# Optimization experiments

Hardware: AMD Instinct MI355X
Metric: run time of the kernel (lower is better)

Reference implementation:

```python
import jax, jax.numpy as jnp
import numpy as np

DIM = 768   # embedding dim
NH = 12     # num heads
HD = DIM // NH  # head dim = 64
WS = 14     # window size
EPS = 1e-5  # nn.LayerNorm default


def _ln(x, w, b):
    m = jnp.mean(x, -1, keepdims=True)
    v = jnp.var(x, -1, keepdims=True)
    return (x - m) * jax.lax.rsqrt(v + EPS) * w + b


def setup_inputs() -> dict:
    key = jax.random.key(0)
    ks = jax.random.split(key, 8)
    def n(k, shape, s=0.02):
        return jax.random.normal(k, shape, jnp.float32) * s
    return {
        "x": jax.random.normal(ks[0], (4, 64, 64, DIM), jnp.float32),
        "ln1_w": jnp.ones((DIM,), jnp.float32),
        "ln1_b": jnp.zeros((DIM,), jnp.float32),
        "qkv_w": n(ks[1], (DIM, 3 * DIM)),
        "qkv_b": jnp.zeros((3 * DIM,), jnp.float32),
        "proj_w": n(ks[2], (DIM, DIM)),
        "proj_b": jnp.zeros((DIM,), jnp.float32),
        "rel_pos_h": n(ks[3], (2 * WS - 1, HD)),
        "rel_pos_w": n(ks[4], (2 * WS - 1, HD)),
        "ln2_w": jnp.ones((DIM,), jnp.float32),
        "ln2_b": jnp.zeros((DIM,), jnp.float32),
        "fc1_w": n(ks[5], (DIM, 4 * DIM)),
        "fc1_b": jnp.zeros((4 * DIM,), jnp.float32),
        "fc2_w": n(ks[6], (4 * DIM, DIM)),
        "fc2_b": jnp.zeros((DIM,), jnp.float32),
    }


def _block(x, ln1_w, ln1_b, qkv_w, qkv_b, proj_w, proj_b,
           rel_pos_h, rel_pos_w, ln2_w, ln2_b, fc1_w, fc1_b, fc2_w, fc2_b):
    B, H, W, C = x.shape
    shortcut = x
    xn = _ln(x, ln1_w, ln1_b)

    # ---- window partition (pad H,W up to multiples of WS) ----
    pad_h = (-H) % WS
    pad_w = (-W) % WS
    xp = jnp.pad(xn, ((0, 0), (0, pad_h), (0, pad_w), (0, 0)))
    Hp, Wp = H + pad_h, W + pad_w
    nh, nw = Hp // WS, Wp // WS
    xw = xp.reshape(B, nh, WS, nw, WS, C).transpose(0, 1, 3, 2, 4, 5)
    xw = xw.reshape(B * nh * nw, WS, WS, C)  # [Bw, ws, ws, C]
    Bw = B * nh * nw
    N = WS * WS

    # ---- attention with decomposed relative position bias ----
    qkv = xw.reshape(Bw, N, C) @ qkv_w + qkv_b            # [Bw, N, 3C]
    qkv = qkv.reshape(Bw, N, 3, NH, HD).transpose(2, 0, 3, 1, 4)  # [3, Bw, NH, N, HD]
    q, k, v = qkv[0], qkv[1], qkv[2]
    scale = HD ** -0.5
    attn = jnp.einsum("bhnd,bhmd->bhnm", q * scale, k)    # [Bw, NH, N, N]

    # decomposed rel pos: Rh[q_h, k_h, c], Rw[q_w, k_w, c]
    idx = jnp.arange(WS)[:, None] - jnp.arange(WS)[None, :] + (WS - 1)
    Rh = rel_pos_h[idx]  # [ws, ws, HD]
    Rw = rel_pos_w[idx]  # [ws, ws, HD]
    rq = q.reshape(Bw, NH, WS, WS, HD)
    rel_h = jnp.einsum("bnhwc,hkc->bnhwk", rq, Rh)  # over q rows vs k rows
    rel_w = jnp.einsum("bnhwc,wkc->bnhwk", rq, Rw)  # over q cols vs k cols
    attn = (attn.reshape(Bw, NH, WS, WS, WS, WS)
            + rel_h[..., :, None] + rel_w[..., None, :]).reshape(Bw, NH, N, N)

    attn = jax.nn.softmax(attn, axis=-1)
    out = jnp.einsum("bhnm,bhmd->bhnd", attn, v)          # [Bw, NH, N, HD]
    out = out.transpose(0, 2, 1, 3).reshape(Bw, WS, WS, C)
    out = out @ proj_w + proj_b

    # ---- window unpartition + crop padding ----
    out = out.reshape(B, nh, nw, WS, WS, C).transpose(0, 1, 3, 2, 4, 5)
    out = out.reshape(B, Hp, Wp, C)[:, :H, :W, :]

    x = shortcut + out

    # ---- MLP ----
    h = _ln(x, ln2_w, ln2_b)
    h = jax.nn.gelu(h @ fc1_w + fc1_b, approximate=False)
    x = x + (h @ fc2_w + fc2_b)
    return x


def reference(x, ln1_w, ln1_b, qkv_w, qkv_b, proj_w, proj_b,
              rel_pos_h, rel_pos_w, ln2_w, ln2_b, fc1_w, fc1_b, fc2_w, fc2_b):
    return _block(x, ln1_w, ln1_b, qkv_w, qkv_b, proj_w, proj_b,
                  rel_pos_h, rel_pos_w, ln2_w, ln2_b, fc1_w, fc1_b, fc2_w, fc2_b)
```

## Files before the change

kernel.cpp:

```cpp
#include <hip/hip_runtime.h>

typedef unsigned short u16;
typedef __bf16 bf16x8_t __attribute__((ext_vector_type(8)));
typedef float f32x4_t __attribute__((ext_vector_type(4)));

__device__ __forceinline__ float bf2f(u16 u) {
    union { unsigned u; float f; } c; c.u = ((unsigned)u) << 16; return c.f;
}
__device__ __forceinline__ u16 f2bf(float f) {
    union { float f; unsigned u; } c; c.f = f;
    unsigned u = c.u;
    unsigned r = (u + 0x7FFFu + ((u >> 16) & 1u)) >> 16;
    return (u16)r;
}

__device__ __forceinline__ void gld16(const u16* g, u16* l) {
    __builtin_amdgcn_global_load_lds(
        (const __attribute__((address_space(1))) unsigned*)g,
        (__attribute__((address_space(3))) unsigned*)l, 16, 0, 0);
}

__device__ __forceinline__ void block_sum2(float& s, float& sq) {
    for (int o = 32; o > 0; o >>= 1) { s += __shfl_xor(s, o); sq += __shfl_xor(sq, o); }
    __shared__ float sh[8];
    int wid = threadIdx.x >> 6;
    if ((threadIdx.x & 63) == 0) { sh[wid] = s; sh[4 + wid] = sq; }
    __syncthreads();
    s  = sh[0] + sh[1] + sh[2] + sh[3];
    sq = sh[4] + sh[5] + sh[6] + sh[7];
}

__global__ __launch_bounds__(256) void ln1_window(
    const float* __restrict__ x, const float* __restrict__ w, const float* __restrict__ b,
    u16* __restrict__ out, int row0)
{
    int lrow = blockIdx.x, tid = threadIdx.x;
    int wr = row0 + lrow;
    int wb = wr / 196, t = wr % 196;
    int gh = ((wb % 25) / 5) * 14 + t / 14;
    int gw = (wb % 5) * 14 + t % 14;
    size_t orow = (size_t)lrow * 768;
    __shared__ u16 rowbuf[768];
    if (gh >= 64 || gw >= 64) {
        rowbuf[tid] = 0; rowbuf[tid + 256] = 0; rowbuf[tid + 512] = 0;
        __syncthreads();
        if (tid < 96) *(uint4*)&out[orow + (tid << 3)] = *(const uint4*)&rowbuf[tid << 3];
        return;
    }
    size_t base = (size_t)(((wb / 25) * 64 + gh) * 64 + gw) * 768;
    float v0 = x[base + tid], v1 = x[base + tid + 256], v2 = x[base + tid + 512];
    float s = v0 + v1 + v2, sq = v0 * v0 + v1 * v1 + v2 * v2;
    block_sum2(s, sq);
    float mean = s * (1.0f / 768.0f);
    float var  = sq * (1.0f / 768.0f) - mean * mean;
    float inv  = rsqrtf(var + 1e-5f);
    rowbuf[tid]       = f2bf((v0 - mean) * inv * w[tid]       + b[tid]);
    rowbuf[tid + 256] = f2bf((v1 - mean) * inv * w[tid + 256] + b[tid + 256]);
    rowbuf[tid + 512] = f2bf((v2 - mean) * inv * w[tid + 512] + b[tid + 512]);
    __syncthreads();
    if (tid < 96) *(uint4*)&out[orow + (tid << 3)] = *(const uint4*)&rowbuf[tid << 3];
}

__global__ __launch_bounds__(256) void ln2_chunk(
    const float* __restrict__ xin, const float* __restrict__ w, const float* __restrict__ b,
    u16* __restrict__ out)
{
    int row = blockIdx.x, tid = threadIdx.x;
    size_t base = (size_t)row * 768;
    __shared__ u16 rowbuf[768];
    float v0 = xin[base + tid], v1 = xin[base + tid + 256], v2 = xin[base + tid + 512];
    float s = v0 + v1 + v2, sq = v0 * v0 + v1 * v1 + v2 * v2;
    block_sum2(s, sq);
    float mean = s * (1.0f / 768.0f);
    float var  = sq * (1.0f / 768.0f) - mean * mean;
    float inv  = rsqrtf(var + 1e-5f);
    rowbuf[tid]       = f2bf((v0 - mean) * inv * w[tid]       + b[tid]);
    rowbuf[tid + 256] = f2bf((v1 - mean) * inv * w[tid + 256] + b[tid + 256]);
    rowbuf[tid + 512] = f2bf((v2 - mean) * inv * w[tid + 512] + b[tid + 512]);
    __syncthreads();
    if (tid < 96) *(uint4*)&out[base + (tid << 3)] = *(const uint4*)&rowbuf[tid << 3];
}

__global__ __launch_bounds__(256) void transpose_wf(
    const float* __restrict__ in, u16* __restrict__ out, int K, int N)
{
    __shared__ u16 t[32][33];
    __shared__ u16 tt[32][32];
    int n0 = blockIdx.x * 32, k0 = blockIdx.y * 32;
    int tx = threadIdx.x & 31, ty = threadIdx.x >> 5;
    for (int q = 0; q < 4; q++) {
        int k = k0 + ty + q * 8, n = n0 + tx;
        t[ty + q * 8][tx] = (k < K && n < N) ? f2bf(in[(size_t)k * N + n]) : (u16)0;
    }
    __syncthreads();
    for (int q = 0; q < 4; q++) tt[ty + q * 8][tx] = t[tx][ty + q * 8];
    __syncthreads();
    if (threadIdx.x < 128) {
        int r = threadIdx.x >> 2, c8 = (threadIdx.x & 3) << 3;
        int n = n0 + r, k = k0 + c8;
        if (n < N && k < K)
            *(uint4*)&out[(size_t)n * K + k] = *(const uint4*)&tt[r][c8];
    }
}

__global__ __launch_bounds__(256) void build_relT(
    const float* __restrict__ rh, const float* __restrict__ rw, u16* __restrict__ out)
{
    int i = blockIdx.x * 256 + threadIdx.x;
    int r = i >> 6, c = i & 63;
    float v = (r < 27) ? rh[r * 64 + c] : (r < 54 ? rw[(r - 27) * 64 + c] : 0.f);
    out[i] = f2bf(v);
}

__global__ __launch_bounds__(256) void build_vt(
    const u16* __restrict__ qkvc, u16* __restrict__ vt)
{
    int z = blockIdx.x;
    int wb = z / 12, h = z % 12;
    __shared__ u16 t[64][232];
    int tid = threadIdx.x;
    for (int base = 0; base < 196; base += 4) {
        int m = base + (tid >> 6);
        int d = tid & 63;
        t[d][m] = qkvc[(size_t)(wb * 196 + m) * 2304 + 1536 + h * 64 + d];
    }
    for (int idx = tid; idx < 28 * 64; idx += 256) {
        int m = 196 + idx / 64, d = idx % 64;
        t[d][m] = 0;
    }
    __syncthreads();
    size_t ob = (size_t)z * 64 * 224;
    for (int idx = tid; idx < 64 * 28; idx += 256) {
        int d = idx / 28, c8 = (idx % 28) << 3;
        *(uint4*)&vt[ob + (size_t)d * 224 + c8] = *(const uint4*)&t[d][c8];
    }
}

__global__ __launch_bounds__(256) void softmax_rel2(
    u16* __restrict__ S, const u16* __restrict__ G2)
{
    int z = blockIdx.y;
    int wv = threadIdx.x >> 6, lane = threadIdx.x & 63;
    int n = blockIdx.x * 4 + wv;
    size_t srow = (size_t)z * 196 * 224 + (size_t)n * 224;
    const u16* g2 = G2 + (size_t)z * 196 * 64 + (size_t)n * 64;
    int qh = n / 14, qw = n % 14;
    float s[4];
    for (int c = 0; c < 4; c++) {
        int m = c * 64 + lane;
        if (m < 196) {
            int kk = m / 14, jj = m % 14;
            float bh = bf2f(g2[qh - kk + 13]);
            float bw = bf2f(g2[27 + qw - jj + 13]);
            s[c] = 0.125f * bf2f(S[srow + m]) + bh + bw;
        } else s[c] = -1e30f;
    }
    float mx = fmaxf(fmaxf(s[0], s[1]), fmaxf(s[2], s[3]));
    for (int o = 32; o > 0; o >>= 1) mx = fmaxf(mx, __shfl_xor(mx, o));
    float e[4], sm = 0.f;
    for (int c = 0; c < 4; c++) {
        int m = c * 64 + lane;
        e[c] = (m < 196) ? expf(s[c] - mx) : 0.f;
        sm += e[c];
    }
    for (int o = 32; o > 0; o >>= 1) sm += __shfl_xor(sm, o);
    float inv = 1.0f / sm;
    for (int c = 0; c < 4; c++) {
        int m = c * 64 + lane;
        if (m < 224) S[srow + m] = f2bf(e[c] * inv);
    }
}

__device__ __forceinline__ int swz_off(int row, int kcElem) {
    return row * 32 + (kcElem ^ (((row >> 1) & 3) << 3));
}

template <int MODE>
__global__ __launch_bounds__(256, 4) void gemm_nt(
    const u16* __restrict__ Aall, const u16* __restrict__ Ball,
    const float* __restrict__ bias, const float* xf,
    u16* __restrict__ Cb, float* Cf, int M, int row0)
{
    constexpr int BK = 32;
    int N, K, lda, ldb;
    size_t aoff = 0, boff = 0, coff = 0;
    if constexpr (MODE == 0) { N = 2304; K = 768; lda = 768; ldb = 768; }
    else if constexpr (MODE == 1) {
        N = 196; K = 64; lda = 2304; ldb = 2304;
        int z = blockIdx.z;
        aoff = (size_t)(z / 12) * 196 * 2304 + (size_t)(z % 12) * 64;
        boff = aoff + 768;
        coff = (size_t)z * 196 * 224;
    } else if constexpr (MODE == 2) {
        N = 64; K = 224; lda = 224; ldb = 224;
        int z = blockIdx.z;
        aoff = (size_t)z * 196 * 224;
        boff = (size_t)z * 64 * 224;
        coff = (size_t)(z / 12) * 196 * 768 + (size_t)(z % 12) * 64;
    } else if constexpr (MODE == 3) { N = 768; K = 768; lda = 768; ldb = 768; }
    else if constexpr (MODE == 4) { N = 3072; K = 768; lda = 768; ldb = 768; }
    else if constexpr (MODE == 6) {
        N = 64; K = 64; lda = 2304; ldb = 64;
        int z = blockIdx.z;
        aoff = (size_t)(z / 12) * 196 * 2304 + (size_t)(z % 12) * 64;
        boff = 0;
        coff = (size_t)z * 196 * 64;
    }
    else { N = 768; K = 3072; lda = 3072; ldb = 3072; }

    __shared__ __align__(16) u16 smem[16384];

    int tid = threadIdx.x, wid = tid >> 6, lane = tid & 63;
    int quad = lane >> 4, l16 = lane & 15;

    int bx = blockIdx.x, by = blockIdx.y;
    if constexpr (MODE != 1 && MODE != 2 && MODE != 6) {
        int gX = gridDim.x;
        int nwg = gX * gridDim.y;
        int orig = by * gX + bx;
        int q = nwg >> 3, r = nwg & 7;
        int xcd = orig & 7, idx = orig >> 3;
        int wg = (xcd < r ? xcd * (q + 1) : r * (q + 1) + (xcd - r) * q) + idx;
        bx = wg % gX; by = wg / gX;
    }
    int m_tile = by * 128, n_tile = bx * 128;
    int wm0 = (wid >> 1) * 64, wn0 = (wid & 1) * 64;

    const u16* A = Aall + aoff;
    const u16* B = Ball + boff;

    const u16* gA[2]; const u16* gB[2];
    int loff[2];
    {
        int s = lane & 3, rofs = lane >> 2;
        for (int j = 0; j < 2; j++) {
            int r0 = wid * 32 + j * 16;
            int rr = r0 + rofs;
            int xr = (rr >> 1) & 3;
            int colo = ((s ^ xr) << 3);
            int am = m_tile + rr; if (am > M - 1) am = M - 1;
            int bn = n_tile + rr; if (bn > N - 1) bn = N - 1;
            gA[j] = A + (size_t)am * lda + colo;
            gB[j] = B + (size_t)bn * ldb + colo;
            loff[j] = r0 * 32;
        }
    }

    f32x4_t acc[4][4];
    f32x4_t z4 = {0.f, 0.f, 0.f, 0.f};
    for (int mt = 0; mt < 4; mt++)
        for (int nt = 0; nt < 4; nt++) acc[mt][nt] = z4;

    for (int j = 0; j < 2; j++) {
        gld16(gA[j], smem + loff[j]);
        gld16(gB[j], smem + 4096 + loff[j]);
    }

    int cur = 0;
    for (int k0 = 0; k0 < K; k0 += BK) {
        __syncthreads();
        int boffc = cur << 13;
        if (k0 + BK < K) {
            int boffn = boffc ^ 8192;
            for (int j = 0; j < 2; j++) {
                gld16(gA[j] + k0 + BK, smem + boffn + loff[j]);
                gld16(gB[j] + k0 + BK, smem + boffn + 4096 + loff[j]);
            }
        }
        const u16* Ac = smem + boffc;
        const u16* Bc = smem + boffc + 4096;
        bf16x8_t af[4], bfv[4];
        for (int t = 0; t < 4; t++) {
            int ar = wm0 + t * 16 + l16;
            int br = wn0 + t * 16 + l16;
            af[t]  = *(const bf16x8_t*)&Ac[swz_off(ar, quad * 8)];
            bfv[t] = *(const bf16x8_t*)&Bc[swz_off(br, quad * 8)];
        }
        for (int mt = 0; mt < 4; mt++)
            for (int nt = 0; nt < 4; nt++)
                acc[mt][nt] = __builtin_amdgcn_mfma_f32_16x16x32_bf16(
                    af[mt], bfv[nt], acc[mt][nt], 0, 0, 0);
        cur ^= 1;
    }

    if constexpr (MODE == 0 || MODE == 1 || MODE == 2 || MODE == 4 || MODE == 6) {
        u16* Cs = smem;
        int ldc = (MODE == 0) ? 2304 : (MODE == 1) ? 224 : (MODE == 2) ? 768
                : (MODE == 6) ? 64 : 3072;
        int colmax = (MODE == 1) ? 224 : N;
        for (int half = 0; half < 2; half++) {
            __syncthreads();
            if ((wm0 >> 6) == half) {
                for (int mt = 0; mt < 4; mt++) {
                    int rl = mt * 16 + quad * 4;
                    for (int nt = 0; nt < 4; nt++) {
                        int cl = wn0 + nt * 16 + l16;
                        int col = n_tile + cl;
                        for (int rg = 0; rg < 4; rg++) {
                            float v = acc[mt][nt][rg];
                            u16 o;
                            if constexpr (MODE == 0) o = f2bf(v + bias[col]);
                            else if constexpr (MODE == 4) {
                                float g = v + bias[col];
                                o = f2bf(0.5f * g * (1.0f + erff(g * 0.70710678118f)));
                            } else o = f2bf(v);
                            Cs[(rl + rg) * 136 + cl] = o;
                        }
                    }
                }
            }
            __syncthreads();
            for (int it = 0; it < 4; it++) {
                int chunk = tid + it * 256;
                int r = chunk >> 4, c8 = (chunk & 15) << 3;
                int grow = m_tile + half * 64 + r, gcol = n_tile + c8;
                if (grow >= M || gcol >= colmax) continue;
                *(uint4*)&Cb[coff + (size_t)grow * ldc + gcol] =
                    *(const uint4*)&Cs[r * 136 + c8];
            }
        }
    } else {
        float* Cfs = (float*)smem;
        for (int q = 0; q < 4; q++) {
            __syncthreads();
            if ((wm0 >> 6) == (q >> 1)) {
                for (int mt2 = 0; mt2 < 2; mt2++) {
                    int mt = (q & 1) * 2 + mt2;
                    int rloc = mt2 * 16 + quad * 4;
                    for (int nt = 0; nt < 4; nt++) {
                        int cl = wn0 + nt * 16 + l16;
                        for (int rg = 0; rg < 4; rg++)
                            Cfs[(rloc + rg) * 132 + cl] = acc[mt][nt][rg];
                    }
                }
            }
            __syncthreads();
            for (int it = 0; it < 4; it++) {
                int chunk = tid + it * 256;
                int r = chunk >> 5, c4 = (chunk & 31) << 2;
                int grow = m_tile + q * 32 + r;
                int gcol = n_tile + c4;
                if (grow >= M || gcol >= N) continue;
                f32x4_t v4 = *(const f32x4_t*)&Cfs[r * 132 + c4];
                f32x4_t b4 = *(const f32x4_t*)&bias[gcol];
                if constexpr (MODE == 5) {
                    size_t idx = (size_t)(row0 + grow) * 768 + gcol;
                    f32x4_t x4 = *(const f32x4_t*)&xf[idx];
                    f32x4_t o4;
                    for (int j = 0; j < 4; j++) o4[j] = v4[j] + x4[j] + b4[j];
                    *(f32x4_t*)&Cf[idx] = o4;
                } else {
                    int wr = row0 + grow;
                    int wb2 = wr / 196, t2 = wr % 196;
                    int gh = ((wb2 % 25) / 5) * 14 + t2 / 14;
                    int gw = (wb2 % 5) * 14 + t2 % 14;
                    if (gh < 64 && gw < 64) {
                        size_t g = (size_t)(((wb2 / 25) * 64 + gh) * 64 + gw) * 768 + gcol;
                        f32x4_t x4 = *(const f32x4_t*)&xf[g];
                        f32x4_t o4;
                        for (int j = 0; j < 4; j++) o4[j] = v4[j] + x4[j] + b4[j];
                        *(f32x4_t*)&Cf[g] = o4;
                    }
                }
            }
        }
    }
}

extern "C" void kernel_launch(void* const* d_in, const int* in_sizes, int n_in,
                              void* d_out, int out_size, void* d_ws, size_t ws_size,
                              hipStream_t stream)
{
    (void)in_sizes; (void)n_in; (void)out_size;
    const float* x      = (const float*)d_in[0];
    const float* ln1_w  = (const float*)d_in[1];
    const float* ln1_b  = (const float*)d_in[2];
    const float* qkv_w  = (const float*)d_in[3];
    const float* qkv_b  = (const float*)d_in[4];
    const float* proj_w = (const float*)d_in[5];
    const float* proj_b = (const float*)d_in[6];
    const float* rel_h  = (const float*)d_in[7];
    const float* rel_w  = (const float*)d_in[8];
    const float* ln2_w  = (const float*)d_in[9];
    const float* ln2_b  = (const float*)d_in[10];
    const float* fc1_w  = (const float*)d_in[11];
    const float* fc1_b  = (const float*)d_in[12];
    const float* fc2_w  = (const float*)d_in[13];
    const float* fc2_b  = (const float*)d_in[14];

    const size_t WT = 14155776ull + 8192ull;
    char* ws = (char*)d_ws;
    u16* qkvT  = (u16*)ws;
    u16* projT = qkvT + 2304 * 768;
    u16* fc1T  = projT + 768 * 768;
    u16* fc2T  = fc1T + 3072 * 768;
    u16* relT  = fc2T + 3072 * 768;
    char* scratch = ws + WT;
    size_t avail = (ws_size > WT) ? (ws_size - WT) : 0;

    const size_t perW = 3204096ull;
    static const int wc_cand[8] = {100, 50, 25, 20, 10, 5, 2, 1};
    int Wc = 1;
    for (int i = 0; i < 8; i++) {
        if ((size_t)wc_cand[i] * perW <= avail) { Wc = wc_cand[i]; break; }
    }
    static const int rm_cand[8] = {16384, 8192, 4096, 2048, 1024, 512, 256, 128};
    int Rm = 128;
    for (int i = 0; i < 8; i++) {
        if ((size_t)rm_cand[i] * 7680ull <= avail) { Rm = rm_cand[i]; break; }
    }

    u16* lnwc  = (u16*)scratch;
    u16* qkvc  = (u16*)(scratch + (size_t)Wc * 301056ull);
    u16* Sc    = (u16*)(scratch + (size_t)Wc * 1204224ull);
    u16* vtc   = (u16*)(scratch + (size_t)Wc * 2257920ull);
    u16* attnc = (u16*)(scratch + (size_t)Wc * 2601984ull);
    u16* G2c   = (u16*)(scratch + (size_t)Wc * 2903040ull);
    u16* hbuf  = (u16*)scratch;
    u16* xn2c  = (u16*)(scratch + (size_t)Rm * 6144ull);
    float* dout = (float*)d_out;

    transpose_wf<<<dim3(72, 24), 256, 0, stream>>>(qkv_w, qkvT, 768, 2304);
    transpose_wf<<<dim3(24, 24), 256, 0, stream>>>(proj_w, projT, 768, 768);
    transpose_wf<<<dim3(96, 24), 256, 0, stream>>>(fc1_w, fc1T, 768, 3072);
    transpose_wf<<<dim3(24, 96), 256, 0, stream>>>(fc2_w, fc2T, 3072, 768);
    build_relT<<<16, 256, 0, stream>>>(rel_h, rel_w, relT);

    int nch = 100 / Wc;
    int rows = Wc * 196;
    int gy = (rows + 127) / 128;
    for (int c = 0; c < nch; c++) {
        int r0 = c * rows;
        ln1_window<<<rows, 256, 0, stream>>>(x, ln1_w, ln1_b, lnwc, r0);
        gemm_nt<0><<<dim3(18, gy), 256, 0, stream>>>(
            lnwc, qkvT, qkv_b, nullptr, qkvc, nullptr, rows, 0);
        gemm_nt<1><<<dim3(2, 2, Wc * 12), 256, 0, stream>>>(
            qkvc, qkvc, nullptr, nullptr, Sc, nullptr, 196, 0);
        gemm_nt<6><<<dim3(1, 2, Wc * 12), 256, 0, stream>>>(
            qkvc, relT, nullptr, nullptr, G2c, nullptr, 196, 0);
        build_vt<<<Wc * 12, 256, 0, stream>>>(qkvc, vtc);
        softmax_rel2<<<dim3(49, Wc * 12), 256, 0, stream>>>(Sc, G2c);
        gemm_nt<2><<<dim3(1, 2, Wc * 12), 256, 0, stream>>>(
            Sc, vtc, nullptr, nullptr, attnc, nullptr, 196, 0);
        gemm_nt<3><<<dim3(6, gy), 256, 0, stream>>>(
            attnc, projT, proj_b, x, nullptr, dout, rows, r0);
    }

    int nm = 16384 / Rm;
    for (int c = 0; c < nm; c++) {
        int r0 = c * Rm;
        ln2_chunk<<<Rm, 256, 0, stream>>>(dout + (size_t)r0 * 768, ln2_w, ln2_b, xn2c);
        gemm_nt<4><<<dim3(24, Rm / 128), 256, 0, stream>>>(
            xn2c, fc1T, fc1_b, nullptr, hbuf, nullptr, Rm, 0);
        gemm_nt<5><<<dim3(6, Rm / 128), 256, 0, stream>>>(
            hbuf, fc2T, fc2_b, dout, nullptr, dout, Rm, r0);
    }
}
```

Measured before the change: 754.1 us.

## Triple-buffer GEMM K-loop with explicit vmcnt waits and raw barriers

Changes the shared GEMM kernel from a two-stage to a three-stage LDS pipeline. It prefetches two K-tiles ahead and waits with s_waitcnt vmcnt(4) instead of draining all loads before each barrier. The aim is to hide global-to-LDS load latency behind the MFMA work. In exchange, LDS grows from 32KB to 48KB per block and launch bounds drop to 3 blocks per CU, which lowers occupancy. The hand-written vmcnt counts and raw s_barrier also carry a risk of races if the compiler issues other memory ops.

```diff
diff --git a/kernel.cpp b/kernel.cpp
--- a/kernel.cpp
+++ b/kernel.cpp
@@ -176,7 +176,7 @@
 }
 
 template <int MODE>
-__global__ __launch_bounds__(256, 4) void gemm_nt(
+__global__ __launch_bounds__(256, 3) void gemm_nt(
     const u16* __restrict__ Aall, const u16* __restrict__ Ball,
     const float* __restrict__ bias, const float* xf,
     u16* __restrict__ Cb, float* Cf, int M, int row0)
@@ -208,7 +208,7 @@
     }
     else { N = 768; K = 3072; lda = 3072; ldb = 3072; }
 
-    __shared__ __align__(16) u16 smem[16384];
+    __shared__ __align__(16) u16 smem[24576];
 
     int tid = threadIdx.x, wid = tid >> 6, lane = tid & 63;
     int quad = lane >> 4, l16 = lane & 15;
@@ -251,24 +251,37 @@
     for (int mt = 0; mt < 4; mt++)
         for (int nt = 0; nt < 4; nt++) acc[mt][nt] = z4;
 
+    int nsteps = K / BK;
     for (int j = 0; j < 2; j++) {
         gld16(gA[j], smem + loff[j]);
         gld16(gB[j], smem + 4096 + loff[j]);
     }
+    for (int j = 0; j < 2; j++) {
+        gld16(gA[j] + BK, smem + 8192 + loff[j]);
+        gld16(gB[j] + BK, smem + 12288 + loff[j]);
+    }
 
     int cur = 0;
-    for (int k0 = 0; k0 < K; k0 += BK) {
-        __syncthreads();
-        int boffc = cur << 13;
-        if (k0 + BK < K) {
-            int boffn = boffc ^ 8192;
+    for (int k = 0; k < nsteps; k++) {
+        if (k + 1 < nsteps) {
+            asm volatile("s_waitcnt vmcnt(4)" ::: "memory");
+        } else {
+            asm volatile("s_waitcnt vmcnt(0)" ::: "memory");
+        }
+        __builtin_amdgcn_sched_barrier(0);
+        __builtin_amdgcn_s_barrier();
+        __builtin_amdgcn_sched_barrier(0);
+        if (k + 2 < nsteps) {
+            int nb = cur + 2; if (nb >= 3) nb -= 3;
+            u16* dst = smem + nb * 8192;
+            int kn = (k + 2) * BK;
             for (int j = 0; j < 2; j++) {
-                gld16(gA[j] + k0 + BK, smem + boffn + loff[j]);
-                gld16(gB[j] + k0 + BK, smem + boffn + 4096 + loff[j]);
+                gld16(gA[j] + kn, dst + loff[j]);
+                gld16(gB[j] + kn, dst + 4096 + loff[j]);
             }
         }
-        const u16* Ac = smem + boffc;
-        const u16* Bc = smem + boffc + 4096;
+        const u16* Ac = smem + cur * 8192;
+        const u16* Bc = Ac + 4096;
         bf16x8_t af[4], bfv[4];
         for (int t = 0; t < 4; t++) {
             int ar = wm0 + t * 16 + l16;
@@ -280,7 +293,7 @@
             for (int nt = 0; nt < 4; nt++)
                 acc[mt][nt] = __builtin_amdgcn_mfma_f32_16x16x32_bf16(
                     af[mt], bfv[nt], acc[mt][nt], 0, 0, 0);
-        cur ^= 1;
+        cur++; if (cur >= 3) cur -= 3;
     }
 
     if constexpr (MODE == 0 || MODE == 1 || MODE == 2 || MODE == 4 || MODE == 6) {
```

New measurement: 753.3 us. No clear change (-0.1%).
